# Kernel optimization log

Hardware: AMD Instinct MI355X
Metric: run time of the kernel (lower is better)

## Reference

```python
import jax, jax.numpy as jnp
import numpy as np

ALPHA = 0.5
BETA = 0.5


def _attend(qk, feat, W, wp, b):
    """One additive co-attention stage.
    qk:   (B, K)     projected query
    feat: (B, N, D)  keys/values
    W:    (D, K), wp: (2K, 1), b: (N,)
    returns (B, D) attention-weighted sum of feat.
    """
    proj = jnp.einsum('bnd,dk->bnk', feat, W)                    # (B,N,K)
    q = jnp.broadcast_to(qk[:, None, :], proj.shape)             # repeat query
    H = jnp.tanh(jnp.concatenate([q, proj], axis=-1))            # (B,N,2K)
    logits = jnp.einsum('bnk,k->bn', H, wp[:, 0]) + b            # (B,N)
    P = jax.nn.softmax(logits, axis=-1)
    return jnp.einsum('bn,bnd->bd', P, feat)                     # (B,D)


def setup_inputs() -> dict:
    key = jax.random.key(0)
    B, R, S, G, E, D, K = 256, 49, 128, 20, 30, 1024, 256
    ks = jax.random.split(key, 19)
    w = lambda k, shp: 0.05 * jax.random.normal(k, shp, jnp.float32)
    return {
        'ifeature_h': jax.random.normal(ks[0], (B, R, D), jnp.float32),
        'tfeature_h': jax.random.normal(ks[1], (B, S, D), jnp.float32),
        'cfeature':   jax.random.normal(ks[2], (B, G, D), jnp.float32),
        'efeature':   jax.random.normal(ks[3], (B, E, D), jnp.float32),
        'w_Vit_0':  w(ks[4],  (D, K)),
        'w_Vc_0':   w(ks[5],  (D, K)),
        'w_Pc_0':   w(ks[6],  (2 * K, 1)),
        'b_Pc_0':   jnp.zeros((G,), jnp.float32),
        'w_Ve_0':   w(ks[7],  (D, K)),
        'w_Pe_0':   w(ks[8],  (2 * K, 1)),
        'b_Pe_0':   jnp.zeros((E,), jnp.float32),
        'w_Vi_1':   w(ks[9],  (D, K)),
        'w_Vtce_1': w(ks[10], (D, K)),
        'w_Pi_1':   w(ks[11], (2 * K, 1)),
        'b_Pi_1':   jnp.zeros((R,), jnp.float32),
        'w_Vice_2': w(ks[12], (D, K)),
        'w_Vt_2':   w(ks[13], (D, K)),
        'w_Pt_2':   w(ks[14], (2 * K, 1)),
        'b_Pt_2':   jnp.zeros((S,), jnp.float32),
    }


def reference(ifeature_h, tfeature_h, cfeature, efeature,
              w_Vit_0, w_Vc_0, w_Pc_0, b_Pc_0,
              w_Ve_0, w_Pe_0, b_Pe_0,
              w_Vi_1, w_Vtce_1, w_Pi_1, b_Pi_1,
              w_Vice_2, w_Vt_2, w_Pt_2, b_Pt_2):
    ifeat = jnp.mean(ifeature_h, axis=1)   # (B, D)
    tfeat = jnp.mean(tfeature_h, axis=1)   # (B, D)

    # stage 0: image+text query attends over caption group and title
    q0 = (ifeat + tfeat) @ w_Vit_0                               # (B, K)
    Vc = _attend(q0, cfeature, w_Vc_0, w_Pc_0, b_Pc_0)           # (B, D)
    Ve = _attend(q0, efeature, w_Ve_0, w_Pe_0, b_Pe_0)           # (B, D)

    # stage 1: text+caption+title query attends over image regions
    q1 = (tfeat + ALPHA * Vc + BETA * Ve) @ w_Vtce_1
    Vi = _attend(q1, ifeature_h, w_Vi_1, w_Pi_1, b_Pi_1)

    # stage 2: image+caption+title query attends over text tokens
    q2 = (Vi + ALPHA * Vc + BETA * Ve) @ w_Vice_2
    Vt = _attend(q2, tfeature_h, w_Vt_2, w_Pt_2, b_Pt_2)

    return Vi + Vt + ALPHA * Vc + BETA * Ve
```

## Files before the change

### kernel.cpp

```cpp
#include <hip/hip_runtime.h>
#include <hip/hip_bf16.h>
#include <stdint.h>


#define D_DIM 1024
#define K_OUT 256
#define BM 128
#define BK 64

typedef float f32x4 __attribute__((ext_vector_type(4)));
typedef short bf16x8 __attribute__((ext_vector_type(8)));
typedef unsigned short u16x8 __attribute__((ext_vector_type(8)));

static __device__ __forceinline__ unsigned short f2bf(float f) {
    return __builtin_bit_cast(unsigned short, __float2bfloat16(f));
}

static __device__ __forceinline__ float fast_tanh(float x) {
    float e = __expf(2.0f * x);
    return 1.0f - 2.0f / (e + 1.0f);
}

__global__ __launch_bounds__(256) void convert_wt(
    const float* __restrict__ w_c, const float* __restrict__ w_e,
    const float* __restrict__ w_i, const float* __restrict__ w_t,
    unsigned short* __restrict__ wt_all)
{
    const float* wsel[4] = {w_c, w_e, w_i, w_t};
    const float* W = wsel[blockIdx.x];
    unsigned short* Wt = wt_all + (size_t)blockIdx.x * (K_OUT * D_DIM);
    const int d0 = blockIdx.y * 32;

    __shared__ float tile[32][K_OUT];
    const int t = threadIdx.x;
    for (int i = 0; i < 32; ++i) {
        int idx = t + i * 256;
        int dd = idx >> 8, n = idx & 255;
        tile[dd][n] = W[(size_t)(d0 + dd) * K_OUT + n];
    }
    __syncthreads();
    unsigned short buf[32];
#pragma unroll
    for (int dd = 0; dd < 32; ++dd) buf[dd] = f2bf(tile[dd][t]);
#pragma unroll
    for (int i = 0; i < 4; ++i) {
        u16x8 v;
#pragma unroll
        for (int j = 0; j < 8; ++j) v[j] = buf[i * 8 + j];
        *reinterpret_cast<u16x8*>(&Wt[(size_t)t * D_DIM + d0 + i * 8]) = v;
    }
}

struct GemmStage {
    const float* feat;
    const unsigned short* wt;
    const float* wp;
    float* s_out;
    int blk_start;
};

__global__ __launch_bounds__(512) void logits_gemm(
    GemmStage g0, GemmStage g1, GemmStage g2, GemmStage g3)
{
    __shared__ __align__(16) unsigned char AsRaw[BM * 128];
    __shared__ __align__(16) unsigned char WsRaw[K_OUT * 128];
    __shared__ float wp2s[K_OUT];
    __shared__ float partial[BM][4];

    GemmStage st;
    const int bid = blockIdx.x;
    if (bid < g1.blk_start) st = g0;
    else if (bid < g2.blk_start) st = g1;
    else if (bid < g3.blk_start) st = g2;
    else st = g3;
    const int m0 = (bid - st.blk_start) * BM;

    const int t = threadIdx.x;
    if (t < K_OUT) wp2s[t] = st.wp[K_OUT + t];

    const int ar = t >> 2, ac2 = t & 3;
    const int wr = t >> 3, wc = t & 7;
    const int wv = t >> 6, lane = t & 63;
    const int wm = wv >> 2, wn = wv & 3;
    const int q = lane >> 4, c16 = lane & 15;
    const int xa = c16 & 7;

    f32x4 acc[4][4];
#pragma unroll
    for (int i = 0; i < 4; ++i)
#pragma unroll
        for (int j = 0; j < 4; ++j) acc[i][j] = (f32x4){0.f, 0.f, 0.f, 0.f};

    const float* aptr = st.feat + (size_t)(m0 + ar) * D_DIM + ac2 * 16;
    const unsigned short* wptr = st.wt + (size_t)wr * D_DIM + wc * 8;
    const int ab0 = ar * 128 + ((((ac2 * 2)    ) ^ (ar & 7)) << 4);
    const int ab1 = ar * 128 + ((((ac2 * 2) + 1) ^ (ar & 7)) << 4);

#pragma unroll 1
    for (int kt = 0; kt < D_DIM / BK; ++kt) {
        const int d0 = kt * BK;
        __syncthreads();
        {
            f32x4 v0 = *reinterpret_cast<const f32x4*>(aptr + d0);
            f32x4 v1 = *reinterpret_cast<const f32x4*>(aptr + d0 + 4);
            f32x4 v2 = *reinterpret_cast<const f32x4*>(aptr + d0 + 8);
            f32x4 v3 = *reinterpret_cast<const f32x4*>(aptr + d0 + 12);
            u16x8 o0, o1;
#pragma unroll
            for (int j = 0; j < 4; ++j) {
                o0[j]     = f2bf(v0[j]); o0[4 + j] = f2bf(v1[j]);
                o1[j]     = f2bf(v2[j]); o1[4 + j] = f2bf(v3[j]);
            }
            *reinterpret_cast<u16x8*>(&AsRaw[ab0]) = o0;
            *reinterpret_cast<u16x8*>(&AsRaw[ab1]) = o1;
        }
#pragma unroll
        for (int i = 0; i < 4; ++i) {
            const int n = wr + i * 64;
            u16x8 v = *reinterpret_cast<const u16x8*>(wptr + (size_t)i * 64 * D_DIM + d0);
            const int bb = n * 128 + ((wc ^ (n & 7)) << 4);
            *reinterpret_cast<u16x8*>(&WsRaw[bb]) = v;
        }
        __syncthreads();
#pragma unroll
        for (int ks = 0; ks < 2; ++ks) {
            bf16x8 af[4], bfr[4];
            const int ck = (((ks * 4 + q) ^ xa)) << 4;
#pragma unroll
            for (int mt = 0; mt < 4; ++mt) {
                const int row = wm * 64 + mt * 16 + c16;
                af[mt] = *reinterpret_cast<const bf16x8*>(&AsRaw[row * 128 + ck]);
            }
#pragma unroll
            for (int nt = 0; nt < 4; ++nt) {
                const int row = wn * 64 + nt * 16 + c16;
                bfr[nt] = *reinterpret_cast<const bf16x8*>(&WsRaw[row * 128 + ck]);
            }
#pragma unroll
            for (int mt = 0; mt < 4; ++mt)
#pragma unroll
                for (int nt = 0; nt < 4; ++nt)
                    acc[mt][nt] = __builtin_amdgcn_mfma_f32_16x16x32_bf16(
                        af[mt], bfr[nt], acc[mt][nt], 0, 0, 0);
        }
    }

#pragma unroll
    for (int mt = 0; mt < 4; ++mt) {
#pragma unroll
        for (int r = 0; r < 4; ++r) {
            float v = 0.f;
#pragma unroll
            for (int nt = 0; nt < 4; ++nt) {
                const int col = wn * 64 + nt * 16 + c16;
                v += fast_tanh(acc[mt][nt][r]) * wp2s[col];
            }
            v += __shfl_xor(v, 1);
            v += __shfl_xor(v, 2);
            v += __shfl_xor(v, 4);
            v += __shfl_xor(v, 8);
            if (c16 == 0) partial[wm * 64 + mt * 16 + q * 4 + r][wn] = v;
        }
    }
    __syncthreads();
    if (t < BM)
        st.s_out[m0 + t] = partial[t][0] + partial[t][1] + partial[t][2] + partial[t][3];
}

struct PVStage {
    const float* s;
    const float* bias;
    const float* feat;
    float* v_out;
    int N;
};

__global__ __launch_bounds__(256) void softmax_pv(
    PVStage p0, PVStage p1, PVStage p2, PVStage p3)
{
    PVStage st = (blockIdx.y == 0) ? p0 : (blockIdx.y == 1) ? p1
               : (blockIdx.y == 2) ? p2 : p3;
    const int b = blockIdx.x, t = threadIdx.x;
    const int N = st.N;

    __shared__ float P[128];
    __shared__ float inv_s;

    if (t < N) P[t] = st.s[b * N + t] + st.bias[t];
    __syncthreads();
    if (t < 64) {
        float m = -3.4e38f;
        for (int n = t; n < N; n += 64) m = fmaxf(m, P[n]);
#pragma unroll
        for (int sh = 32; sh; sh >>= 1) m = fmaxf(m, __shfl_xor(m, sh));
        float ssum = 0.f;
        for (int n = t; n < N; n += 64) { float e = __expf(P[n] - m); P[n] = e; ssum += e; }
#pragma unroll
        for (int sh = 32; sh; sh >>= 1) ssum += __shfl_xor(ssum, sh);
        if (t == 0) inv_s = 1.0f / ssum;
    }
    __syncthreads();
    const float inv = inv_s;

    f32x4 accv = (f32x4){0.f, 0.f, 0.f, 0.f};
    const float* fb = st.feat + (size_t)b * N * D_DIM + t * 4;
    for (int n = 0; n < N; ++n) {
        f32x4 f = *reinterpret_cast<const f32x4*>(fb + (size_t)n * D_DIM);
        accv += (P[n] * inv) * f;
    }
    *reinterpret_cast<f32x4*>(&st.v_out[(size_t)b * D_DIM + t * 4]) = accv;
}

__global__ __launch_bounds__(256) void combine_out(
    const float* __restrict__ vc, const float* __restrict__ ve,
    const float* __restrict__ vi, const float* __restrict__ vt,
    float* __restrict__ out)
{
    const int i = (blockIdx.x * 256 + threadIdx.x) * 4;
    f32x4 a = *reinterpret_cast<const f32x4*>(vi + i);
    f32x4 bb = *reinterpret_cast<const f32x4*>(vt + i);
    f32x4 c = *reinterpret_cast<const f32x4*>(vc + i);
    f32x4 e = *reinterpret_cast<const f32x4*>(ve + i);
    *reinterpret_cast<f32x4*>(out + i) = a + bb + 0.5f * c + 0.5f * e;
}

extern "C" void kernel_launch(void* const* d_in, const int* in_sizes, int n_in,
                              void* d_out, int out_size, void* d_ws, size_t ws_size,
                              hipStream_t stream)
{
    const float* ifeature = (const float*)d_in[0];
    const float* tfeature = (const float*)d_in[1];
    const float* cfeature = (const float*)d_in[2];
    const float* efeature = (const float*)d_in[3];
    const float* w_Vc = (const float*)d_in[5];
    const float* w_Pc = (const float*)d_in[6];
    const float* b_Pc = (const float*)d_in[7];
    const float* w_Ve = (const float*)d_in[8];
    const float* w_Pe = (const float*)d_in[9];
    const float* b_Pe = (const float*)d_in[10];
    const float* w_Vi = (const float*)d_in[11];
    const float* w_Pi = (const float*)d_in[13];
    const float* b_Pi = (const float*)d_in[14];
    const float* w_Vt = (const float*)d_in[16];
    const float* w_Pt = (const float*)d_in[17];
    const float* b_Pt = (const float*)d_in[18];

    char* ws = (char*)d_ws;
    unsigned short* wt = (unsigned short*)ws;
    float* s_c = (float*)(ws + 2u * 1024 * 1024);
    float* s_e = s_c + 5120;
    float* s_i = s_e + 7680;
    float* s_t = s_i + 12544;
    float* v_c = (float*)(ws + 3u * 1024 * 1024);
    float* v_e = v_c + 256 * 1024;
    float* v_i = v_e + 256 * 1024;
    float* v_t = v_i + 256 * 1024;

    convert_wt<<<dim3(4, 32), 256, 0, stream>>>(w_Vc, w_Ve, w_Vi, w_Vt, wt);

    GemmStage g0{cfeature, wt + 0 * (K_OUT * D_DIM), w_Pc, s_c, 0};
    GemmStage g1{efeature, wt + 1 * (K_OUT * D_DIM), w_Pe, s_e, 40};
    GemmStage g2{ifeature, wt + 2 * (K_OUT * D_DIM), w_Pi, s_i, 100};
    GemmStage g3{tfeature, wt + 3 * (K_OUT * D_DIM), w_Pt, s_t, 198};
    logits_gemm<<<454, 512, 0, stream>>>(g0, g1, g2, g3);

    PVStage p0{s_c, b_Pc, cfeature, v_c, 20};
    PVStage p1{s_e, b_Pe, efeature, v_e, 30};
    PVStage p2{s_i, b_Pi, ifeature, v_i, 49};
    PVStage p3{s_t, b_Pt, tfeature, v_t, 128};
    softmax_pv<<<dim3(256, 4), 256, 0, stream>>>(p0, p1, p2, p3);

    combine_out<<<256, 256, 0, stream>>>(v_c, v_e, v_i, v_t, (float*)d_out);
}
```

Baseline: 98.27 us.

## Split logits GEMM along K_OUT into two halves to double block count

Each logits GEMM block now computes only half of the 256 projection columns, and the grid grows from 454 to 908 blocks. Each half writes its partial tanh-weighted logit sum to a separate buffer, and softmax_pv adds the two partials. The goal is better occupancy across the MI355X CUs and lower per-block register and LDS use. The cost is that every fp32 feature tile is read from memory and converted to bf16 twice.

```diff
diff --git a/kernel.cpp b/kernel.cpp
--- a/kernel.cpp
+++ b/kernel.cpp
@@ -6,7 +6,9 @@
 #define D_DIM 1024
 #define K_OUT 256
 #define BM 128
+#define BN 128
 #define BK 64
+#define NT (D_DIM / BK)
 
 typedef float f32x4 __attribute__((ext_vector_type(4)));
 typedef short bf16x8 __attribute__((ext_vector_type(8)));
@@ -57,47 +59,54 @@
     const float* wp;
     float* s_out;
     int blk_start;
+    int mtiles;
 };
 
 __global__ __launch_bounds__(512) void logits_gemm(
     GemmStage g0, GemmStage g1, GemmStage g2, GemmStage g3)
 {
     __shared__ __align__(16) unsigned char AsRaw[BM * 128];
-    __shared__ __align__(16) unsigned char WsRaw[K_OUT * 128];
-    __shared__ float wp2s[K_OUT];
+    __shared__ __align__(16) unsigned char WsRaw[BN * 128];
+    __shared__ float wp2s[BN];
     __shared__ float partial[BM][4];
 
+    const int bid = blockIdx.x;
+    const int bid2 = bid >> 1, half = bid & 1;
     GemmStage st;
-    const int bid = blockIdx.x;
-    if (bid < g1.blk_start) st = g0;
-    else if (bid < g2.blk_start) st = g1;
-    else if (bid < g3.blk_start) st = g2;
+    if (bid2 < g1.blk_start) st = g0;
+    else if (bid2 < g2.blk_start) st = g1;
+    else if (bid2 < g3.blk_start) st = g2;
     else st = g3;
-    const int m0 = (bid - st.blk_start) * BM;
+    const int m0 = (bid2 - st.blk_start) * BM;
+    const int M = st.mtiles * BM;
+    const int n0 = half * BN;
+    float* sout = st.s_out + (size_t)half * M;
 
     const int t = threadIdx.x;
-    if (t < K_OUT) wp2s[t] = st.wp[K_OUT + t];
+    if (t < BN) wp2s[t] = st.wp[K_OUT + n0 + t];
 
     const int ar = t >> 2, ac2 = t & 3;
-    const int wr = t >> 3, wc = t & 7;
+    const int wr = t >> 2, wc = t & 3;
     const int wv = t >> 6, lane = t & 63;
     const int wm = wv >> 2, wn = wv & 3;
     const int q = lane >> 4, c16 = lane & 15;
     const int xa = c16 & 7;
 
-    f32x4 acc[4][4];
+    f32x4 acc[4][2];
 #pragma unroll
     for (int i = 0; i < 4; ++i)
 #pragma unroll
-        for (int j = 0; j < 4; ++j) acc[i][j] = (f32x4){0.f, 0.f, 0.f, 0.f};
+        for (int j = 0; j < 2; ++j) acc[i][j] = (f32x4){0.f, 0.f, 0.f, 0.f};
 
     const float* aptr = st.feat + (size_t)(m0 + ar) * D_DIM + ac2 * 16;
-    const unsigned short* wptr = st.wt + (size_t)wr * D_DIM + wc * 8;
+    const unsigned short* wptr = st.wt + (size_t)(n0 + wr) * D_DIM + wc * 8;
     const int ab0 = ar * 128 + ((((ac2 * 2)    ) ^ (ar & 7)) << 4);
     const int ab1 = ar * 128 + ((((ac2 * 2) + 1) ^ (ar & 7)) << 4);
+    const int wb0 = wr * 128 + (((wc    ) ^ (wr & 7)) << 4);
+    const int wb1 = wr * 128 + (((wc + 4) ^ (wr & 7)) << 4);
 
 #pragma unroll 1
-    for (int kt = 0; kt < D_DIM / BK; ++kt) {
+    for (int kt = 0; kt < NT; ++kt) {
         const int d0 = kt * BK;
         __syncthreads();
         {
@@ -114,17 +123,16 @@
             *reinterpret_cast<u16x8*>(&AsRaw[ab0]) = o0;
             *reinterpret_cast<u16x8*>(&AsRaw[ab1]) = o1;
         }
-#pragma unroll
-        for (int i = 0; i < 4; ++i) {
-            const int n = wr + i * 64;
-            u16x8 v = *reinterpret_cast<const u16x8*>(wptr + (size_t)i * 64 * D_DIM + d0);
-            const int bb = n * 128 + ((wc ^ (n & 7)) << 4);
-            *reinterpret_cast<u16x8*>(&WsRaw[bb]) = v;
+        {
+            u16x8 v0 = *reinterpret_cast<const u16x8*>(wptr + d0);
+            u16x8 v1 = *reinterpret_cast<const u16x8*>(wptr + d0 + 32);
+            *reinterpret_cast<u16x8*>(&WsRaw[wb0]) = v0;
+            *reinterpret_cast<u16x8*>(&WsRaw[wb1]) = v1;
         }
         __syncthreads();
 #pragma unroll
         for (int ks = 0; ks < 2; ++ks) {
-            bf16x8 af[4], bfr[4];
+            bf16x8 af[4], bfr[2];
             const int ck = (((ks * 4 + q) ^ xa)) << 4;
 #pragma unroll
             for (int mt = 0; mt < 4; ++mt) {
@@ -132,14 +140,14 @@
                 af[mt] = *reinterpret_cast<const bf16x8*>(&AsRaw[row * 128 + ck]);
             }
 #pragma unroll
-            for (int nt = 0; nt < 4; ++nt) {
-                const int row = wn * 64 + nt * 16 + c16;
+            for (int nt = 0; nt < 2; ++nt) {
+                const int row = wn * 32 + nt * 16 + c16;
                 bfr[nt] = *reinterpret_cast<const bf16x8*>(&WsRaw[row * 128 + ck]);
             }
 #pragma unroll
             for (int mt = 0; mt < 4; ++mt)
 #pragma unroll
-                for (int nt = 0; nt < 4; ++nt)
+                for (int nt = 0; nt < 2; ++nt)
                     acc[mt][nt] = __builtin_amdgcn_mfma_f32_16x16x32_bf16(
                         af[mt], bfr[nt], acc[mt][nt], 0, 0, 0);
         }
@@ -151,8 +159,8 @@
         for (int r = 0; r < 4; ++r) {
             float v = 0.f;
 #pragma unroll
-            for (int nt = 0; nt < 4; ++nt) {
-                const int col = wn * 64 + nt * 16 + c16;
+            for (int nt = 0; nt < 2; ++nt) {
+                const int col = wn * 32 + nt * 16 + c16;
                 v += fast_tanh(acc[mt][nt][r]) * wp2s[col];
             }
             v += __shfl_xor(v, 1);
@@ -164,7 +172,7 @@
     }
     __syncthreads();
     if (t < BM)
-        st.s_out[m0 + t] = partial[t][0] + partial[t][1] + partial[t][2] + partial[t][3];
+        sout[m0 + t] = partial[t][0] + partial[t][1] + partial[t][2] + partial[t][3];
 }
 
 struct PVStage {
@@ -182,11 +190,12 @@
                : (blockIdx.y == 2) ? p2 : p3;
     const int b = blockIdx.x, t = threadIdx.x;
     const int N = st.N;
+    const int M = 256 * N;
 
     __shared__ float P[128];
     __shared__ float inv_s;
 
-    if (t < N) P[t] = st.s[b * N + t] + st.bias[t];
+    if (t < N) P[t] = st.s[b * N + t] + st.s[M + b * N + t] + st.bias[t];
     __syncthreads();
     if (t < 64) {
         float m = -3.4e38f;
@@ -248,9 +257,9 @@
     char* ws = (char*)d_ws;
     unsigned short* wt = (unsigned short*)ws;
     float* s_c = (float*)(ws + 2u * 1024 * 1024);
-    float* s_e = s_c + 5120;
-    float* s_i = s_e + 7680;
-    float* s_t = s_i + 12544;
+    float* s_e = s_c + 2 * 5120;
+    float* s_i = s_e + 2 * 7680;
+    float* s_t = s_i + 2 * 12544;
     float* v_c = (float*)(ws + 3u * 1024 * 1024);
     float* v_e = v_c + 256 * 1024;
     float* v_i = v_e + 256 * 1024;
@@ -258,11 +267,11 @@
 
     convert_wt<<<dim3(4, 32), 256, 0, stream>>>(w_Vc, w_Ve, w_Vi, w_Vt, wt);
 
-    GemmStage g0{cfeature, wt + 0 * (K_OUT * D_DIM), w_Pc, s_c, 0};
-    GemmStage g1{efeature, wt + 1 * (K_OUT * D_DIM), w_Pe, s_e, 40};
-    GemmStage g2{ifeature, wt + 2 * (K_OUT * D_DIM), w_Pi, s_i, 100};
-    GemmStage g3{tfeature, wt + 3 * (K_OUT * D_DIM), w_Pt, s_t, 198};
-    logits_gemm<<<454, 512, 0, stream>>>(g0, g1, g2, g3);
+    GemmStage g0{cfeature, wt + 0 * (K_OUT * D_DIM), w_Pc, s_c, 0,   40};
+    GemmStage g1{efeature, wt + 1 * (K_OUT * D_DIM), w_Pe, s_e, 40,  60};
+    GemmStage g2{ifeature, wt + 2 * (K_OUT * D_DIM), w_Pi, s_i, 100, 98};
+    GemmStage g3{tfeature, wt + 3 * (K_OUT * D_DIM), w_Pt, s_t, 198, 256};
+    logits_gemm<<<908, 512, 0, stream>>>(g0, g1, g2, g3);
 
     PVStage p0{s_c, b_Pc, cfeature, v_c, 20};
     PVStage p1{s_e, b_Pe, efeature, v_e, 30};
```

After: 137.9 us. 1.4x slower.

## Replace LDS-tiled logits GEMM with per-wave streaming 32x32 MFMA kernel

Applied to the files above, without the earlier changes.

The weight conversion now writes bf16 weights pre-swizzled into the MFMA 32x32x16 fragment order, so the logits kernel can load both operands directly from global memory into registers without LDS staging or block barriers. Each wave handles a 32-row tile against all 256 output columns, keeping 8 f32x16 accumulators, and fuses tanh and the wp dot product with shuffle reductions. This removes shared-memory traffic and synchronisation but relies on global/L2 bandwidth for repeated weight reads, since each wave streams the full 512 KB weight matrix, and it uses more registers per thread.

```diff
diff --git a/kernel.cpp b/kernel.cpp
--- a/kernel.cpp
+++ b/kernel.cpp
@@ -5,10 +5,9 @@
 
 #define D_DIM 1024
 #define K_OUT 256
-#define BM 128
-#define BK 64
 
 typedef float f32x4 __attribute__((ext_vector_type(4)));
+typedef float f32x16 __attribute__((ext_vector_type(16)));
 typedef short bf16x8 __attribute__((ext_vector_type(8)));
 typedef unsigned short u16x8 __attribute__((ext_vector_type(8)));
 
@@ -24,147 +23,88 @@
 __global__ __launch_bounds__(256) void convert_wt(
     const float* __restrict__ w_c, const float* __restrict__ w_e,
     const float* __restrict__ w_i, const float* __restrict__ w_t,
-    unsigned short* __restrict__ wt_all)
+    unsigned short* __restrict__ wtf)
 {
     const float* wsel[4] = {w_c, w_e, w_i, w_t};
     const float* W = wsel[blockIdx.x];
-    unsigned short* Wt = wt_all + (size_t)blockIdx.x * (K_OUT * D_DIM);
-    const int d0 = blockIdx.y * 32;
-
-    __shared__ float tile[32][K_OUT];
+    unsigned short* out = wtf + (size_t)blockIdx.x * (K_OUT * D_DIM);
+    const int kb = blockIdx.y;
     const int t = threadIdx.x;
-    for (int i = 0; i < 32; ++i) {
-        int idx = t + i * 256;
-        int dd = idx >> 8, n = idx & 255;
-        tile[dd][n] = W[(size_t)(d0 + dd) * K_OUT + n];
-    }
-    __syncthreads();
-    unsigned short buf[32];
-#pragma unroll
-    for (int dd = 0; dd < 32; ++dd) buf[dd] = f2bf(tile[dd][t]);
-#pragma unroll
-    for (int i = 0; i < 4; ++i) {
-        u16x8 v;
-#pragma unroll
-        for (int j = 0; j < 8; ++j) v[j] = buf[i * 8 + j];
-        *reinterpret_cast<u16x8*>(&Wt[(size_t)t * D_DIM + d0 + i * 8]) = v;
-    }
-}
-
-struct GemmStage {
-    const float* feat;
-    const unsigned short* wt;
-    const float* wp;
-    float* s_out;
-    int blk_start;
-};
-
-__global__ __launch_bounds__(512) void logits_gemm(
-    GemmStage g0, GemmStage g1, GemmStage g2, GemmStage g3)
-{
-    __shared__ __align__(16) unsigned char AsRaw[BM * 128];
-    __shared__ __align__(16) unsigned char WsRaw[K_OUT * 128];
-    __shared__ float wp2s[K_OUT];
-    __shared__ float partial[BM][4];
-
-    GemmStage st;
-    const int bid = blockIdx.x;
-    if (bid < g1.blk_start) st = g0;
-    else if (bid < g2.blk_start) st = g1;
-    else if (bid < g3.blk_start) st = g2;
-    else st = g3;
-    const int m0 = (bid - st.blk_start) * BM;
-
-    const int t = threadIdx.x;
-    if (t < K_OUT) wp2s[t] = st.wp[K_OUT + t];
-
-    const int ar = t >> 2, ac2 = t & 3;
-    const int wr = t >> 3, wc = t & 7;
-    const int wv = t >> 6, lane = t & 63;
-    const int wm = wv >> 2, wn = wv & 3;
-    const int q = lane >> 4, c16 = lane & 15;
-    const int xa = c16 & 7;
-
-    f32x4 acc[4][4];
-#pragma unroll
-    for (int i = 0; i < 4; ++i)
-#pragma unroll
-        for (int j = 0; j < 4; ++j) acc[i][j] = (f32x4){0.f, 0.f, 0.f, 0.f};
-
-    const float* aptr = st.feat + (size_t)(m0 + ar) * D_DIM + ac2 * 16;
-    const unsigned short* wptr = st.wt + (size_t)wr * D_DIM + wc * 8;
-    const int ab0 = ar * 128 + ((((ac2 * 2)    ) ^ (ar & 7)) << 4);
-    const int ab1 = ar * 128 + ((((ac2 * 2) + 1) ^ (ar & 7)) << 4);
-
-#pragma unroll 1
-    for (int kt = 0; kt < D_DIM / BK; ++kt) {
-        const int d0 = kt * BK;
-        __syncthreads();
-        {
-            f32x4 v0 = *reinterpret_cast<const f32x4*>(aptr + d0);
-            f32x4 v1 = *reinterpret_cast<const f32x4*>(aptr + d0 + 4);
-            f32x4 v2 = *reinterpret_cast<const f32x4*>(aptr + d0 + 8);
-            f32x4 v3 = *reinterpret_cast<const f32x4*>(aptr + d0 + 12);
-            u16x8 o0, o1;
-#pragma unroll
-            for (int j = 0; j < 4; ++j) {
-                o0[j]     = f2bf(v0[j]); o0[4 + j] = f2bf(v1[j]);
-                o1[j]     = f2bf(v2[j]); o1[4 + j] = f2bf(v3[j]);
-            }
-            *reinterpret_cast<u16x8*>(&AsRaw[ab0]) = o0;
-            *reinterpret_cast<u16x8*>(&AsRaw[ab1]) = o1;
-        }
-#pragma unroll
-        for (int i = 0; i < 4; ++i) {
-            const int n = wr + i * 64;
-            u16x8 v = *reinterpret_cast<const u16x8*>(wptr + (size_t)i * 64 * D_DIM + d0);
-            const int bb = n * 128 + ((wc ^ (n & 7)) << 4);
-            *reinterpret_cast<u16x8*>(&WsRaw[bb]) = v;
-        }
-        __syncthreads();
-#pragma unroll
-        for (int ks = 0; ks < 2; ++ks) {
-            bf16x8 af[4], bfr[4];
-            const int ck = (((ks * 4 + q) ^ xa)) << 4;
-#pragma unroll
-            for (int mt = 0; mt < 4; ++mt) {
-                const int row = wm * 64 + mt * 16 + c16;
-                af[mt] = *reinterpret_cast<const bf16x8*>(&AsRaw[row * 128 + ck]);
-            }
-#pragma unroll
-            for (int nt = 0; nt < 4; ++nt) {
-                const int row = wn * 64 + nt * 16 + c16;
-                bfr[nt] = *reinterpret_cast<const bf16x8*>(&WsRaw[row * 128 + ck]);
-            }
-#pragma unroll
-            for (int mt = 0; mt < 4; ++mt)
-#pragma unroll
-                for (int nt = 0; nt < 4; ++nt)
-                    acc[mt][nt] = __builtin_amdgcn_mfma_f32_16x16x32_bf16(
-                        af[mt], bfr[nt], acc[mt][nt], 0, 0, 0);
-        }
-    }
-
-#pragma unroll
-    for (int mt = 0; mt < 4; ++mt) {
-#pragma unroll
-        for (int r = 0; r < 4; ++r) {
-            float v = 0.f;
-#pragma unroll
-            for (int nt = 0; nt < 4; ++nt) {
-                const int col = wn * 64 + nt * 16 + c16;
-                v += fast_tanh(acc[mt][nt][r]) * wp2s[col];
-            }
-            v += __shfl_xor(v, 1);
-            v += __shfl_xor(v, 2);
-            v += __shfl_xor(v, 4);
-            v += __shfl_xor(v, 8);
-            if (c16 == 0) partial[wm * 64 + mt * 16 + q * 4 + r][wn] = v;
-        }
-    }
-    __syncthreads();
-    if (t < BM)
-        st.s_out[m0 + t] = partial[t][0] + partial[t][1] + partial[t][2] + partial[t][3];
+
+    unsigned short tmp[16];
+#pragma unroll
+    for (int j = 0; j < 16; ++j)
+        tmp[j] = f2bf(W[(size_t)(kb * 16 + j) * K_OUT + t]);
+
+    u16x8 lo, hi;
+#pragma unroll
+    for (int j = 0; j < 8; ++j) { lo[j] = tmp[j]; hi[j] = tmp[8 + j]; }
+    unsigned short* dst = out + (size_t)kb * 4096 + t * 16;
+    *reinterpret_cast<u16x8*>(dst) = lo;
+    *reinterpret_cast<u16x8*>(dst + 8) = hi;
+}
+
+__global__ __launch_bounds__(256) void logits_stream(
+    const float* __restrict__ f_c, const float* __restrict__ f_e,
+    const float* __restrict__ f_i, const float* __restrict__ f_t,
+    const unsigned short* __restrict__ wtf,
+    const float* __restrict__ wp_c, const float* __restrict__ wp_e,
+    const float* __restrict__ wp_i, const float* __restrict__ wp_t,
+    float* __restrict__ s_c, float* __restrict__ s_e,
+    float* __restrict__ s_i, float* __restrict__ s_t)
+{
+    const int wv = threadIdx.x >> 6, lane = threadIdx.x & 63;
+    const int rt = blockIdx.x * 4 + wv;
+
+    const float* feat; const unsigned short* wt; const float* wp;
+    float* sout; int m0;
+    if (rt < 160)      { feat = f_c; wt = wtf;          wp = wp_c; sout = s_c; m0 = rt * 32; }
+    else if (rt < 400) { feat = f_e; wt = wtf + 262144; wp = wp_e; sout = s_e; m0 = (rt - 160) * 32; }
+    else if (rt < 792) { feat = f_i; wt = wtf + 524288; wp = wp_i; sout = s_i; m0 = (rt - 400) * 32; }
+    else               { feat = f_t; wt = wtf + 786432; wp = wp_t; sout = s_t; m0 = (rt - 792) * 32; }
+
+    const int l31 = lane & 31, lh = lane >> 5;
+    const float* arow = feat + (size_t)(m0 + l31) * D_DIM + lh * 8;
+    const unsigned short* bbase = wt + (size_t)l31 * 16 + lh * 8;
+
+    f32x16 acc[8];
+#pragma unroll
+    for (int f = 0; f < 8; ++f) acc[f] = (f32x16)(0.f);
+
+#pragma unroll 2
+    for (int kk = 0; kk < 64; ++kk) {
+        f32x4 a0 = *reinterpret_cast<const f32x4*>(arow + kk * 16);
+        f32x4 a1 = *reinterpret_cast<const f32x4*>(arow + kk * 16 + 4);
+        u16x8 bu[8];
+#pragma unroll
+        for (int f = 0; f < 8; ++f)
+            bu[f] = *reinterpret_cast<const u16x8*>(bbase + kk * 4096 + f * 512);
+        u16x8 au;
+#pragma unroll
+        for (int j = 0; j < 4; ++j) { au[j] = f2bf(a0[j]); au[4 + j] = f2bf(a1[j]); }
+        const bf16x8 af = __builtin_bit_cast(bf16x8, au);
+#pragma unroll
+        for (int f = 0; f < 8; ++f)
+            acc[f] = __builtin_amdgcn_mfma_f32_32x32x16_bf16(
+                af, __builtin_bit_cast(bf16x8, bu[f]), acc[f], 0, 0, 0);
+    }
+
+    float wpf[8];
+#pragma unroll
+    for (int f = 0; f < 8; ++f) wpf[f] = wp[K_OUT + f * 32 + l31];
+
+#pragma unroll
+    for (int r = 0; r < 16; ++r) {
+        float v = 0.f;
+#pragma unroll
+        for (int f = 0; f < 8; ++f) v += fast_tanh(acc[f][r]) * wpf[f];
+        v += __shfl_xor(v, 1);
+        v += __shfl_xor(v, 2);
+        v += __shfl_xor(v, 4);
+        v += __shfl_xor(v, 8);
+        v += __shfl_xor(v, 16);
+        if (l31 == 0) sout[m0 + ((r & 3) + 8 * (r >> 2) + 4 * lh)] = v;
+    }
 }
 
 struct PVStage {
@@ -246,7 +186,7 @@
     const float* b_Pt = (const float*)d_in[18];
 
     char* ws = (char*)d_ws;
-    unsigned short* wt = (unsigned short*)ws;
+    unsigned short* wtf = (unsigned short*)ws;
     float* s_c = (float*)(ws + 2u * 1024 * 1024);
     float* s_e = s_c + 5120;
     float* s_i = s_e + 7680;
@@ -256,13 +196,11 @@
     float* v_i = v_e + 256 * 1024;
     float* v_t = v_i + 256 * 1024;
 
-    convert_wt<<<dim3(4, 32), 256, 0, stream>>>(w_Vc, w_Ve, w_Vi, w_Vt, wt);
-
-    GemmStage g0{cfeature, wt + 0 * (K_OUT * D_DIM), w_Pc, s_c, 0};
-    GemmStage g1{efeature, wt + 1 * (K_OUT * D_DIM), w_Pe, s_e, 40};
-    GemmStage g2{ifeature, wt + 2 * (K_OUT * D_DIM), w_Pi, s_i, 100};
-    GemmStage g3{tfeature, wt + 3 * (K_OUT * D_DIM), w_Pt, s_t, 198};
-    logits_gemm<<<454, 512, 0, stream>>>(g0, g1, g2, g3);
+    convert_wt<<<dim3(4, 64), 256, 0, stream>>>(w_Vc, w_Ve, w_Vi, w_Vt, wtf);
+
+    logits_stream<<<454, 256, 0, stream>>>(
+        cfeature, efeature, ifeature, tfeature, wtf,
+        w_Pc, w_Pe, w_Pi, w_Pt, s_c, s_e, s_i, s_t);
 
     PVStage p0{s_c, b_Pc, cfeature, v_c, 20};
     PVStage p1{s_e, b_Pe, efeature, v_e, 30};
```

Result: slower. 161.3 us (+64.1%).
